# Kernel tuning notes

Measured on AMD Instinct MI355X. Metric: run time of the kernel, lower is better.

## Reference

```python
import jax, jax.numpy as jnp
import numpy as np

B, S, HID, NH = 4, 2048, 2048, 16
HD = HID // NH
DECAY_INIT = 0.95


def setup_inputs() -> dict:
    key = jax.random.key(0)
    k1, k2, k3 = jax.random.split(key, 3)
    x = jax.random.normal(k1, (B, S, HID), jnp.float32)
    # torch Linear weights stored as [in, out] for x @ W; scaled like default init
    W_qkv = jax.random.normal(k2, (HID, 3 * HID), jnp.float32) / np.float32(np.sqrt(HID))
    W_out = jax.random.normal(k3, (HID, HID), jnp.float32) / np.float32(np.sqrt(HID))
    decay_param = jnp.full((NH,), DECAY_INIT, jnp.float32)
    kv0 = jnp.zeros((B, NH, HD), jnp.float32)
    k_sum0 = jnp.zeros((B, NH, HD), jnp.float32)
    attention_mask = jnp.ones((B, 1, 1, S), jnp.float32)
    return dict(x=x, kv0=kv0, k_sum0=k_sum0, attention_mask=attention_mask,
                W_qkv=W_qkv, W_out=W_out, decay_param=decay_param)


def _phi(u):
    # kernel feature map: elu(x) + 1 (non-negative)
    return jax.nn.elu(u) + 1.0


def reference(x, kv0, k_sum0, attention_mask, W_qkv, W_out, decay_param):
    b, s, hid = x.shape
    nh = decay_param.shape[0]
    hd = hid // nh
    qkv = x @ W_qkv                               # [b, s, 3*hid]
    q, k, v = jnp.split(qkv, 3, axis=-1)

    def to_time_major(t):                         # [b, s, hid] -> [s, b, nh, hd]
        return t.reshape(b, s, nh, hd).transpose(1, 0, 2, 3)

    q = _phi(to_time_major(q))
    k = _phi(to_time_major(k))
    v = to_time_major(v)

    # mask [b,1,1,s] -> [s, b, 1, 1]; padded tokens don't update the state
    m = attention_mask.reshape(b, 1, s, 1).transpose(2, 0, 1, 3)
    k = k * m
    v = v * m

    decay = jax.nn.sigmoid(decay_param)[None, :, None]  # [1, nh, 1]

    def step(carry, inp):
        kv, ks = carry                             # each [b, nh, hd]
        q_t, k_t, v_t = inp                        # each [b, nh, hd]
        kv = decay * kv + k_t * v_t
        ks = decay * ks + k_t
        num = jnp.sum(q_t * kv, axis=-1, keepdims=True)
        den = jnp.maximum(jnp.sum(q_t * ks, axis=-1, keepdims=True), 1e-6)
        return (kv, ks), (num / den) * q_t

    (kv, ks), outs = jax.lax.scan(step, (kv0, k_sum0), (q, k, v))
    out = outs.transpose(1, 0, 2, 3).reshape(b, s, hid) @ W_out
    return out, kv, ks
```

## Files before the change

kernel.cpp:

```cpp
#include <hip/hip_runtime.h>
#include <hip/hip_bf16.h>

typedef __hip_bfloat16 bf16;
typedef short bf16x8 __attribute__((ext_vector_type(8)));
typedef float f32x4 __attribute__((ext_vector_type(4)));

#define BB   4
#define SS   2048
#define HID  2048
#define NHD  16
#define HD   128
#define NCH  64
#define CHL  32

__device__ inline float sigm(float x) { return 1.f / (1.f + __expf(-x)); }
__device__ inline float phi_f(float v) { return v > 0.f ? v + 1.f : __expf(v); }

__device__ inline int probe_fp32(const void* probe) {
    return ((const unsigned*)probe)[0] != 0x3F733F73u;
}
__device__ inline float ldd(const void* p, int fp32, size_t i) {
    return fp32 ? ((const float*)p)[i] : __bfloat162float(((const bf16*)p)[i]);
}
__device__ inline void st_dual(void* p, int fp32, size_t i, float v) {
    if (fp32) ((float*)p)[i] = v;
    else      ((bf16*)p)[i] = __float2bfloat16(v);
}

__device__ inline void ld2(const bf16* p, float& a, float& b) {
    unsigned u = *(const unsigned*)p;
    union U { unsigned x; float f; } lo, hi;
    lo.x = u << 16; hi.x = u & 0xffff0000u;
    a = lo.f; b = hi.f;
}
__device__ inline void st2(bf16* p, float a, float b) {
    __hip_bfloat162 v;
    v.x = __float2bfloat16(a);
    v.y = __float2bfloat16(b);
    *(__hip_bfloat162*)p = v;
}

__device__ __forceinline__ void gload_lds16(const bf16* g, bf16* l) {
    __builtin_amdgcn_global_load_lds((const __attribute__((address_space(1))) void*)g,
                                     (__attribute__((address_space(3))) void*)l,
                                     16, 0, 0);
}

#define NB_CVT 16384
#define NB_T1  3072
#define NB_T2  1024
__global__ __launch_bounds__(256) void prep(const void* __restrict__ x,
                                            bf16* __restrict__ x_bf,
                                            const void* __restrict__ Wqkv,
                                            bf16* __restrict__ WqkvT,
                                            const void* __restrict__ Wout,
                                            bf16* __restrict__ WoutT,
                                            const void* __restrict__ probe) {
    int fp32 = probe_fp32(probe);
    int bid = blockIdx.x;
    int tid = threadIdx.x;
    if (bid < NB_CVT) {
        size_t i = ((size_t)bid * 256 + tid) * 4;
        if (fp32) {
            float4 v = *(const float4*)((const float*)x + i);
            bf16* o = x_bf + i;
            o[0] = __float2bfloat16(v.x); o[1] = __float2bfloat16(v.y);
            o[2] = __float2bfloat16(v.z); o[3] = __float2bfloat16(v.w);
        } else {
            *(short4*)(x_bf + i) = *(const short4*)((const bf16*)x + i);
        }
        return;
    }
    const void* in; bf16* out; int R, C, idx;
    if (bid < NB_CVT + NB_T1) {
        in = Wqkv; out = WqkvT; R = HID; C = 3 * HID; idx = bid - NB_CVT;
    } else {
        in = Wout; out = WoutT; R = HID; C = HID; idx = bid - NB_CVT - NB_T1;
    }
    int ctiles = C / 64;
    int c0 = (idx % ctiles) * 64;
    int r0 = (idx / ctiles) * 64;
    __shared__ bf16 t[64][65];
    int c = tid & 63;
    int rb = tid >> 6;
#pragma unroll
    for (int i = 0; i < 16; i++) {
        int r = rb + i * 4;
        t[r][c] = __float2bfloat16(ldd(in, fp32, (size_t)(r0 + r) * C + c0 + c));
    }
    __syncthreads();
#pragma unroll
    for (int i = 0; i < 16; i++) {
        int r = rb + i * 4;
        out[(size_t)(c0 + r) * R + r0 + c] = t[c][r];
    }
}

template <int MH>
__device__ __forceinline__ void lda_frags(const short* ldsA, bf16x8 (&af)[4][2],
                                          int wm2, int l15, int quad, int sw) {
#pragma unroll
    for (int i = 0; i < 4; i++) {
#pragma unroll
        for (int s = 0; s < 2; s++)
            af[i][s] = *(const bf16x8*)&ldsA[(MH * 128 + wm2 + i * 16 + l15) * 64 +
                                             (((quad + 4 * s) ^ sw) << 3)];
    }
}
template <int NH>
__device__ __forceinline__ void ldb_frags(const short* ldsB, bf16x8 (&bfr)[2][2],
                                          int wn2, int l15, int quad, int sw) {
#pragma unroll
    for (int j = 0; j < 2; j++) {
#pragma unroll
        for (int s = 0; s < 2; s++)
            bfr[j][s] = *(const bf16x8*)&ldsB[(NH * 128 + wn2 + j * 16 + l15) * 64 +
                                              (((quad + 4 * s) ^ sw) << 3)];
    }
}
template <int MH, int NH>
__device__ __forceinline__ void mma_quad(f32x4 (&acc)[2][2][4][2],
                                         const bf16x8 (&af)[4][2],
                                         const bf16x8 (&bfr)[2][2]) {
    __builtin_amdgcn_s_setprio(1);
#pragma unroll
    for (int s = 0; s < 2; s++)
#pragma unroll
        for (int i = 0; i < 4; i++)
#pragma unroll
            for (int j = 0; j < 2; j++)
                acc[MH][NH][i][j] = __builtin_amdgcn_mfma_f32_16x16x32_bf16(
                    af[i][s], bfr[j][s], acc[MH][NH][i][j], 0, 0, 0);
    __builtin_amdgcn_s_setprio(0);
}

template <int EPI>
__global__ __launch_bounds__(512) void gemm256(const bf16* __restrict__ A,
                                               const bf16* __restrict__ Bt,
                                               void* __restrict__ Cv,
                                               const void* __restrict__ mask,
                                               const void* __restrict__ probe,
                                               int M, int N, int K) {
    int fp32 = probe_fp32(probe);
    __shared__ __align__(16) short lds[2][2][256 * 64];
    const int tid = threadIdx.x;
    const int lane = tid & 63, wave = tid >> 6;
    const int quad = lane >> 4, l15 = lane & 15;
    const int sw = l15 & 7;
    const int wm2 = ((wave >> 2) & 1) * 64;
    const int wn2 = (wave & 3) * 32;

    const int nwgx = gridDim.x;
    int wg = blockIdx.y * nwgx + blockIdx.x;
    const int chunk = (nwgx * gridDim.y) >> 3;
    wg = (wg & 7) * chunk + (wg >> 3);
    const int m0 = (wg / nwgx) * 256, n0 = (wg % nwgx) * 256;

    const int KT = K >> 6;

    const int rl = lane >> 3, pu = lane & 7;
    const bf16* gAb = A  + (size_t)(m0 + wave * 8 + rl) * K + ((pu ^ rl) << 3);
    const bf16* gBb = Bt + (size_t)(n0 + wave * 8 + rl) * K + ((pu ^ rl) << 3);

    auto stageA = [&](int bufi, int h, int kt) {
        if (kt >= KT) return;
        const bf16* g = gAb + (size_t)(h * 128) * K + kt * 64;
        gload_lds16(g,                  (bf16*)&lds[bufi][0][(h * 128 + wave * 8) * 64]);
        gload_lds16(g + (size_t)64 * K, (bf16*)&lds[bufi][0][(h * 128 + 64 + wave * 8) * 64]);
    };
    auto stageB = [&](int bufi, int h, int kt) {
        if (kt >= KT) return;
        const bf16* g = gBb + (size_t)(h * 128) * K + kt * 64;
        gload_lds16(g,                  (bf16*)&lds[bufi][1][(h * 128 + wave * 8) * 64]);
        gload_lds16(g + (size_t)64 * K, (bf16*)&lds[bufi][1][(h * 128 + 64 + wave * 8) * 64]);
    };

    f32x4 acc[2][2][4][2];
    f32x4 zero = {0.f, 0.f, 0.f, 0.f};
#pragma unroll
    for (int a = 0; a < 2; a++)
#pragma unroll
        for (int b = 0; b < 2; b++)
#pragma unroll
            for (int i = 0; i < 4; i++)
#pragma unroll
                for (int j = 0; j < 2; j++) acc[a][b][i][j] = zero;
    bf16x8 af[4][2], bfr[2][2];

    stageA(0, 0, 0); stageB(0, 0, 0); stageA(0, 1, 0); stageB(0, 1, 0);
    asm volatile("s_waitcnt vmcnt(4)" ::: "memory");
    stageA(1, 0, 1); stageB(1, 1, 1); stageA(1, 1, 1);
    asm volatile("s_waitcnt vmcnt(6)" ::: "memory");
    __builtin_amdgcn_s_barrier();

#define PH_SYNC_MFMA(MH, NH)                                                   \
    __builtin_amdgcn_sched_barrier(0);                                         \
    __builtin_amdgcn_s_barrier();                                              \
    asm volatile("s_waitcnt lgkmcnt(0)" ::: "memory");                         \
    __builtin_amdgcn_sched_barrier(0);                                         \
    mma_quad<MH, NH>(acc, af, bfr);                                            \
    __builtin_amdgcn_s_barrier();

#define TILE_BODY(BUF, kt)                                                     \
    {                                                                          \
        const short* ldsA = &lds[BUF][0][0];                                   \
        const short* ldsB = &lds[BUF][1][0];                                   \
                    \
        lda_frags<0>(ldsA, af, wm2, l15, quad, sw);                            \
        ldb_frags<0>(ldsB, bfr, wn2, l15, quad, sw);                           \
        stageB((BUF) ^ 1, 0, (kt) + 1);                                        \
        asm volatile("s_waitcnt lgkmcnt(8)" ::: "memory");                     \
        PH_SYNC_MFMA(0, 0)                                                     \
           \
        ldb_frags<1>(ldsB, bfr, wn2, l15, quad, sw);                           \
        stageA((BUF), 0, (kt) + 2);                                            \
        PH_SYNC_MFMA(0, 1)                                                     \
           \
        lda_frags<1>(ldsA, af, wm2, l15, quad, sw);                            \
        stageB((BUF), 1, (kt) + 2);                                            \
        PH_SYNC_MFMA(1, 1)                                                     \
                         \
        ldb_frags<0>(ldsB, bfr, wn2, l15, quad, sw);                           \
        stageA((BUF), 1, (kt) + 2);                                            \
        __builtin_amdgcn_sched_barrier(0);                                     \
        __builtin_amdgcn_s_barrier();                                          \
        asm volatile("s_waitcnt lgkmcnt(0)" ::: "memory");                     \
        __builtin_amdgcn_sched_barrier(0);                                     \
        mma_quad<1, 0>(acc, af, bfr);                                          \
           \
           \
        if ((kt) + 2 < KT) { asm volatile("s_waitcnt vmcnt(6)" ::: "memory"); }\
        else               { asm volatile("s_waitcnt vmcnt(0)" ::: "memory"); }\
        __builtin_amdgcn_s_barrier();                                          \
    }

    for (int kt = 0; kt < KT; kt += 2) {
        TILE_BODY(0, kt)
        TILE_BODY(1, kt + 1)
    }
#undef TILE_BODY
#undef PH_SYNC_MFMA

#pragma unroll
    for (int mh = 0; mh < 2; mh++)
#pragma unroll
        for (int i = 0; i < 4; i++)
#pragma unroll
            for (int r = 0; r < 4; r++) {
                int m = m0 + mh * 128 + wm2 + i * 16 + quad * 4 + r;
                float mk = 1.f;
                if (EPI) mk = ldd(mask, fp32, m);
#pragma unroll
                for (int nh = 0; nh < 2; nh++)
#pragma unroll
                    for (int j = 0; j < 2; j++) {
                        int n = n0 + nh * 128 + wn2 + j * 16 + l15;
                        float v = acc[mh][nh][i][j][r];
                        if (EPI) {
                            if (n < HID)          v = phi_f(v);
                            else if (n < 2 * HID) v = phi_f(v) * mk;
                            else                  v = v * mk;
                            ((bf16*)Cv)[(size_t)m * N + n] = __float2bfloat16(v);
                        } else {
                            st_dual(Cv, fp32, (size_t)m * N + n, v);
                        }
                    }
            }
}

__global__ __launch_bounds__(64) void scan_local(const bf16* __restrict__ qkv,
                                                 float* __restrict__ ckv,
                                                 float* __restrict__ cks,
                                                 const void* __restrict__ decp) {
    int fp32 = probe_fp32(decp);
    int blk = blockIdx.x;
    int bh = blk / NCH, c = blk % NCH;
    int b = bh >> 4, h = bh & 15;
    int lane = threadIdx.x;
    int hd = lane * 2;
    float dec = sigm(ldd(decp, fp32, h));
    const bf16* kb = qkv + (size_t)(b * SS + c * CHL) * (3 * HID) + HID + h * HD + hd;
    const bf16* vb = kb + HID;
    float kv0 = 0.f, kv1 = 0.f, ks0 = 0.f, ks1 = 0.f;
    for (int t = 0; t < CHL; t++) {
        float k0, k1, v0, v1;
        ld2(kb, k0, k1);
        ld2(vb, v0, v1);
        kb += 3 * HID; vb += 3 * HID;
        kv0 = dec * kv0 + k0 * v0;
        kv1 = dec * kv1 + k1 * v1;
        ks0 = dec * ks0 + k0;
        ks1 = dec * ks1 + k1;
    }
    int o = blk * HD + hd;
    ckv[o] = kv0; ckv[o + 1] = kv1;
    cks[o] = ks0; cks[o + 1] = ks1;
}

__global__ __launch_bounds__(64) void scan_out(const bf16* __restrict__ qkv,
                                               const float* __restrict__ ckv,
                                               const float* __restrict__ cks,
                                               const void* __restrict__ kv0in,
                                               const void* __restrict__ ks0in,
                                               const void* __restrict__ decp,
                                               bf16* __restrict__ outs,
                                               void* __restrict__ outbase) {
    int fp32 = probe_fp32(decp);
    int blk = blockIdx.x;
    int bh = blk / NCH, c = blk % NCH;
    int b = bh >> 4, h = bh & 15;
    int lane = threadIdx.x;
    int hd = lane * 2;
    float dec = sigm(ldd(decp, fp32, h));
    float dl = powf(dec, (float)CHL);

    float kva = ldd(kv0in, fp32, bh * HD + hd);
    float kvb = ldd(kv0in, fp32, bh * HD + hd + 1);
    float ksa = ldd(ks0in, fp32, bh * HD + hd);
    float ksb = ldd(ks0in, fp32, bh * HD + hd + 1);
    for (int j = 0; j < c; j++) {
        int o = (bh * NCH + j) * HD + hd;
        kva = dl * kva + ckv[o];
        kvb = dl * kvb + ckv[o + 1];
        ksa = dl * ksa + cks[o];
        ksb = dl * ksb + cks[o + 1];
    }

    const bf16* qb = qkv + (size_t)(b * SS + c * CHL) * (3 * HID) + h * HD + hd;
    const bf16* kb = qb + HID;
    const bf16* vb = qb + 2 * HID;
    bf16* ob = outs + (size_t)(b * SS + c * CHL) * HID + h * HD + hd;
    for (int t = 0; t < CHL; t++) {
        float q0, q1, k0, k1, v0, v1;
        ld2(qb, q0, q1);
        ld2(kb, k0, k1);
        ld2(vb, v0, v1);
        qb += 3 * HID; kb += 3 * HID; vb += 3 * HID;
        kva = dec * kva + k0 * v0;
        kvb = dec * kvb + k1 * v1;
        ksa = dec * ksa + k0;
        ksb = dec * ksb + k1;
        float num = q0 * kva + q1 * kvb;
        float den = q0 * ksa + q1 * ksb;
#pragma unroll
        for (int off = 32; off > 0; off >>= 1) {
            num += __shfl_xor(num, off);
            den += __shfl_xor(den, off);
        }
        float sc = num / fmaxf(den, 1e-6f);
        st2(ob, q0 * sc, q1 * sc);
        ob += HID;
    }

    if (c == NCH - 1) {
        size_t base = (size_t)BB * SS * HID;
        st_dual(outbase, fp32, base + bh * HD + hd, kva);
        st_dual(outbase, fp32, base + bh * HD + hd + 1, kvb);
        st_dual(outbase, fp32, base + BB * NHD * HD + bh * HD + hd, ksa);
        st_dual(outbase, fp32, base + BB * NHD * HD + bh * HD + hd + 1, ksb);
    }
}

extern "C" void kernel_launch(void* const* d_in, const int* in_sizes, int n_in,
                              void* d_out, int out_size, void* d_ws, size_t ws_size,
                              hipStream_t stream) {
    const void* x    = d_in[0];
    const void* kv0  = d_in[1];
    const void* ks0  = d_in[2];
    const void* am   = d_in[3];
    const void* Wqkv = d_in[4];
    const void* Wout = d_in[5];
    const void* decp = d_in[6];

    const int M = BB * SS;
    const int N1 = 3 * HID;
    const int K = HID;

    char* ws = (char*)d_ws;
    bf16* WqkvT = (bf16*)ws;  ws += (size_t)N1 * K * 2;
    bf16* WoutT = (bf16*)ws;  ws += (size_t)HID * HID * 2;
    bf16* x_bf  = (bf16*)ws;  ws += (size_t)M * HID * 2;
    bf16* qkvb  = (bf16*)ws;  ws += (size_t)M * N1 * 2;
    bf16* outs  = (bf16*)ws;  ws += (size_t)M * HID * 2;
    float* ckv  = (float*)ws; ws += (size_t)BB * NHD * NCH * HD * 4;
    float* cks  = (float*)ws; ws += (size_t)BB * NHD * NCH * HD * 4;

    prep<<<NB_CVT + NB_T1 + NB_T2, 256, 0, stream>>>(x, x_bf, Wqkv, WqkvT,
                                                     Wout, WoutT, decp);

    gemm256<1><<<dim3(N1 / 256, M / 256), 512, 0, stream>>>(x_bf, WqkvT, qkvb, am, decp,
                                                            M, N1, K);

    scan_local<<<BB * NHD * NCH, 64, 0, stream>>>(qkvb, ckv, cks, decp);
    scan_out<<<BB * NHD * NCH, 64, 0, stream>>>(qkvb, ckv, cks, kv0, ks0, decp,
                                                outs, d_out);

    gemm256<0><<<dim3(HID / 256, M / 256), 512, 0, stream>>>(outs, WoutT, d_out, nullptr,
                                                             decp, M, HID, K);
}
```

Measured before the change: 497.1 us.

## Keep both B fragment sets in registers and drop grouped workgroup remap in GEMM

The GEMM now holds two B-fragment register sets so the first B fragment is not reloaded from LDS for the last MFMA phase, which removes one LDS read phase and its lgkmcnt wait. Barriers are switched to inline-asm s_barrier with extra sched_barriers so the compiler cannot move code across them. The grouped workgroup-to-tile remapping is replaced with a plain blockIdx mapping. The extra fragments raise VGPR pressure, and losing the remap may hurt L2 reuse between neighbouring tiles.

Result: slower. 508.9 us (+2.4%).

```diff
diff --git a/kernel.cpp b/kernel.cpp
--- a/kernel.cpp
+++ b/kernel.cpp
@@ -45,6 +45,8 @@
                                      (__attribute__((address_space(3))) void*)l,
                                      16, 0, 0);
 }
+
+#define BARE_BARRIER() asm volatile("s_barrier" ::: "memory")
 
 #define NB_CVT 16384
 #define NB_T1  3072
@@ -149,13 +151,7 @@
     const int sw = l15 & 7;
     const int wm2 = ((wave >> 2) & 1) * 64;
     const int wn2 = (wave & 3) * 32;
-
-    const int nwgx = gridDim.x;
-    int wg = blockIdx.y * nwgx + blockIdx.x;
-    const int chunk = (nwgx * gridDim.y) >> 3;
-    wg = (wg & 7) * chunk + (wg >> 3);
-    const int m0 = (wg / nwgx) * 256, n0 = (wg % nwgx) * 256;
-
+    const int m0 = blockIdx.y * 256, n0 = blockIdx.x * 256;
     const int KT = K >> 6;
 
     const int rl = lane >> 3, pu = lane & 7;
@@ -185,21 +181,22 @@
             for (int i = 0; i < 4; i++)
 #pragma unroll
                 for (int j = 0; j < 2; j++) acc[a][b][i][j] = zero;
-    bf16x8 af[4][2], bfr[2][2];
+    bf16x8 af[4][2], bfr0[2][2], bfr1[2][2];
 
     stageA(0, 0, 0); stageB(0, 0, 0); stageA(0, 1, 0); stageB(0, 1, 0);
     asm volatile("s_waitcnt vmcnt(4)" ::: "memory");
     stageA(1, 0, 1); stageB(1, 1, 1); stageA(1, 1, 1);
     asm volatile("s_waitcnt vmcnt(6)" ::: "memory");
-    __builtin_amdgcn_s_barrier();
-
-#define PH_SYNC_MFMA(MH, NH)                                                   \
+    BARE_BARRIER();
+
+#define PH_SYNC_MFMA(MH, NH, BFR)                                              \
     __builtin_amdgcn_sched_barrier(0);                                         \
-    __builtin_amdgcn_s_barrier();                                              \
+    BARE_BARRIER();                                                            \
     asm volatile("s_waitcnt lgkmcnt(0)" ::: "memory");                         \
     __builtin_amdgcn_sched_barrier(0);                                         \
-    mma_quad<MH, NH>(acc, af, bfr);                                            \
-    __builtin_amdgcn_s_barrier();
+    mma_quad<MH, NH>(acc, af, BFR);                                            \
+    __builtin_amdgcn_sched_barrier(0);                                         \
+    BARE_BARRIER();
 
 #define TILE_BODY(BUF, kt)                                                     \
     {                                                                          \
@@ -207,31 +204,30 @@
         const short* ldsB = &lds[BUF][1][0];                                   \
                     \
         lda_frags<0>(ldsA, af, wm2, l15, quad, sw);                            \
-        ldb_frags<0>(ldsB, bfr, wn2, l15, quad, sw);                           \
+        ldb_frags<0>(ldsB, bfr0, wn2, l15, quad, sw);                          \
         stageB((BUF) ^ 1, 0, (kt) + 1);                                        \
         asm volatile("s_waitcnt lgkmcnt(8)" ::: "memory");                     \
-        PH_SYNC_MFMA(0, 0)                                                     \
+        PH_SYNC_MFMA(0, 0, bfr0)                                               \
            \
-        ldb_frags<1>(ldsB, bfr, wn2, l15, quad, sw);                           \
+        ldb_frags<1>(ldsB, bfr1, wn2, l15, quad, sw);                          \
         stageA((BUF), 0, (kt) + 2);                                            \
-        PH_SYNC_MFMA(0, 1)                                                     \
-           \
+        PH_SYNC_MFMA(0, 1, bfr1)                                               \
+                     \
         lda_frags<1>(ldsA, af, wm2, l15, quad, sw);                            \
         stageB((BUF), 1, (kt) + 2);                                            \
-        PH_SYNC_MFMA(1, 1)                                                     \
-                         \
-        ldb_frags<0>(ldsB, bfr, wn2, l15, quad, sw);                           \
+        PH_SYNC_MFMA(1, 1, bfr1)                                               \
+             \
         stageA((BUF), 1, (kt) + 2);                                            \
         __builtin_amdgcn_sched_barrier(0);                                     \
-        __builtin_amdgcn_s_barrier();                                          \
-        asm volatile("s_waitcnt lgkmcnt(0)" ::: "memory");                     \
+        BARE_BARRIER();                                                        \
         __builtin_amdgcn_sched_barrier(0);                                     \
-        mma_quad<1, 0>(acc, af, bfr);                                          \
+        mma_quad<1, 0>(acc, af, bfr0);                                         \
+        __builtin_amdgcn_sched_barrier(0);                                     \
            \
            \
         if ((kt) + 2 < KT) { asm volatile("s_waitcnt vmcnt(6)" ::: "memory"); }\
         else               { asm volatile("s_waitcnt vmcnt(0)" ::: "memory"); }\
-        __builtin_amdgcn_s_barrier();                                          \
+        BARE_BARRIER();                                                        \
     }
 
     for (int kt = 0; kt < KT; kt += 2) {
```
